# Kernel tuning notes

Hardware: AMD Instinct MI355X
Metric: run time of the kernel (lower is better)

Reference implementation:

```python
import jax, jax.numpy as jnp
import numpy as np

N = 200000
H = 128        # n_heads == input feature dim
HID = 512      # hidden_features
D_H = 512      # scaling denominator
C = 10.0       # tanh clip scale


def setup_inputs() -> dict:
    key = jax.random.key(0)
    k0, k1, k2, k3, k4, k5 = jax.random.split(key, 6)
    output = jax.random.normal(k0, (N, H), dtype=jnp.float32)
    # adjacency row: binary mask (which nodes are reachable neighbors)
    adj_modified = (jax.random.uniform(k1, (N,)) < 0.5).astype(jnp.float32)
    W1 = jax.random.normal(k2, (HID, H), dtype=jnp.float32) * (1.0 / np.sqrt(H))
    b1 = jax.random.normal(k3, (HID,), dtype=jnp.float32) * 0.01
    W2 = jax.random.normal(k4, (HID, H), dtype=jnp.float32) * (1.0 / np.sqrt(H))
    b2 = jax.random.normal(k5, (HID,), dtype=jnp.float32) * 0.01
    return {"output": output, "adj_modified": adj_modified,
            "W1": W1, "b1": b1, "W2": W2, "b2": b2, "prev_node": 5}


def reference(output, adj_modified, W1, b1, W2, b2, prev_node):
    # v_i: [1, H] embedding of the previously selected node
    v_i = output[prev_node][None, :]
    # v_j: [N, H] neighbor embeddings gated by the adjacency row
    v_j = adj_modified[:, None] * output
    phi1_v_i = v_i @ W1.T + b1          # [1, HID]
    phi2_v_j = v_j @ W2.T + b2          # [N, HID]
    scores = (phi1_v_i @ phi2_v_j.T) / jnp.sqrt(jnp.asarray(D_H, jnp.float32))  # [1, N]
    attn = C * jnp.tanh(scores) * adj_modified  # clipped + masked, [1, N]
    attn = attn[0]                                # [N]
    w = jax.nn.softmax(attn, axis=0)
    w = w * (attn != 0).astype(w.dtype)
    p = w.max()
    selected_node = jnp.argmax(w)
    return selected_node, p
```

## Files before the change

### kernel.cpp

```cpp
#include <hip/hip_runtime.h>
#include <math.h>

#define H 128
#define HID 512
#define GRID 2048
#define PREP_B 16

struct Ws {
    float sb_part[PREP_B];
    float u_part[PREP_B][H];
    unsigned long long best_part[GRID];
    float Z_part[GRID];
};

__device__ __forceinline__ unsigned int fkey(float f) {
    unsigned int u = __float_as_uint(f);
    return (u & 0x80000000u) ? ~u : (u | 0x80000000u);
}
__device__ __forceinline__ float inv_fkey(unsigned int k) {
    return __uint_as_float((k & 0x80000000u) ? (k ^ 0x80000000u) : ~k);
}

__global__ __launch_bounds__(256)
void prep_kernel(const float* __restrict__ outp, const float* __restrict__ W1,
                 const float* __restrict__ b1, const float* __restrict__ W2,
                 const float* __restrict__ b2, const int* __restrict__ prev,
                 Ws* __restrict__ ws) {
    __shared__ float phi1_s[32];
    __shared__ float sb_s[8];
    __shared__ float u_s[2][H];
    int t = threadIdx.x;
    int lane = t & 63;
    int c = lane & 31;
    int g = t >> 5;
    int kbase = blockIdx.x * 32;
    const float4* vi = (const float4*)(outp + (size_t)prev[0] * H);
    float4 v = vi[c];
    float sb = 0.f;
#pragma unroll
    for (int r = 0; r < 4; ++r) {
        int kl = g * 4 + r;
        int k = kbase + kl;
        float4 w = ((const float4*)(W1 + (size_t)k * H))[c];
        float d = w.x * v.x + w.y * v.y + w.z * v.z + w.w * v.w;
        d += __shfl_xor(d, 16);
        d += __shfl_xor(d, 8);
        d += __shfl_xor(d, 4);
        d += __shfl_xor(d, 2);
        d += __shfl_xor(d, 1);
        if (c == 0) {
            float phi = d + b1[k];
            phi1_s[kl] = phi;
            sb += phi * b2[k];
        }
    }
    if (c == 0) sb_s[g] = sb;
    __syncthreads();
    int h = t & 127;
    int g2 = t >> 7;
    float up = 0.f;
#pragma unroll
    for (int kk = 0; kk < 16; ++kk) {
        int kl = g2 * 16 + kk;
        up += phi1_s[kl] * W2[(size_t)(kbase + kl) * H + h];
    }
    u_s[g2][h] = up;
    __syncthreads();
    if (t < H) ws->u_part[blockIdx.x][t] = u_s[0][t] + u_s[1][t];
    if (t == 0) {
        float s = 0.f;
#pragma unroll
        for (int i = 0; i < 8; ++i) s += sb_s[i];
        ws->sb_part[blockIdx.x] = s;
    }
}

__global__ __launch_bounds__(256)
void score_kernel(const float4* __restrict__ xv, const float* __restrict__ adj,
                  Ws* __restrict__ ws, int n, int ntiles) {
    __shared__ float zs[4];
    __shared__ unsigned long long bs[4];
    const float inv = 0.04419417382415922f;
    int t = threadIdx.x;
    int lane = t & 63;
    int c = lane & 31;
    int hv = lane >> 5;
    int w = t >> 6;
    float4 uv = make_float4(0.f, 0.f, 0.f, 0.f);
    float s_b = 0.f;
#pragma unroll
    for (int b = 0; b < PREP_B; ++b) {
        float4 p = ((const float4*)ws->u_part[b])[c];
        uv.x += p.x; uv.y += p.y; uv.z += p.z; uv.w += p.w;
        s_b += ws->sb_part[b];
    }
    float zloc = 0.f;
    float bscore = -3.4e38f;
    int bidx = -1;
    for (int tile = blockIdx.x; tile < ntiles; tile += GRID) {
        int base = tile * 32 + w * 8 + hv;
        float4 x[4];
#pragma unroll
        for (int r = 0; r < 4; ++r) {
            int row = base + 2 * r;
            if (row >= n) row = n - 1;
            x[r] = xv[(size_t)row * 32 + c];
        }
        float d[4];
#pragma unroll
        for (int r = 0; r < 4; ++r) {
            float dd = x[r].x * uv.x + x[r].y * uv.y + x[r].z * uv.z + x[r].w * uv.w;
            dd += __shfl_xor(dd, 16);
            dd += __shfl_xor(dd, 8);
            dd += __shfl_xor(dd, 4);
            dd += __shfl_xor(dd, 2);
            dd += __shfl_xor(dd, 1);
            d[r] = dd;
        }
        if (c < 4) {
            int row = base + 2 * c;
            if (row < n) {
                float dm = d[0];
#pragma unroll
                for (int r = 1; r < 4; ++r) dm = (c == r) ? d[r] : dm;
                float a = adj[row];
                float attn = 0.f;
                if (a != 0.f) {
                    float score = (s_b + a * dm) * inv;
                    float e = __expf(2.f * score);
                    attn = 10.f * ((e - 1.f) / (e + 1.f));
                    if (score > bscore) { bscore = score; bidx = row; }
                }
                zloc += __expf(attn);
            }
        }
    }
#pragma unroll
    for (int m = 32; m >= 1; m >>= 1) zloc += __shfl_xor(zloc, m);
    unsigned long long pk = 0ull;
    if (bidx >= 0)
        pk = ((unsigned long long)fkey(bscore) << 32) |
             (unsigned long long)(0xFFFFFFFFu - (unsigned int)bidx);
#pragma unroll
    for (int m = 32; m >= 1; m >>= 1) {
        unsigned long long o = __shfl_xor(pk, m);
        if (o > pk) pk = o;
    }
    if (lane == 0) { zs[w] = zloc; bs[w] = pk; }
    __syncthreads();
    if (t == 0) {
        float z = zs[0] + zs[1] + zs[2] + zs[3];
        unsigned long long p2 = bs[0];
#pragma unroll
        for (int i = 1; i < 4; ++i) if (bs[i] > p2) p2 = bs[i];
        ws->Z_part[blockIdx.x] = z;
        ws->best_part[blockIdx.x] = p2;
    }
}

__global__ __launch_bounds__(1024)
void reduce_kernel(const Ws* __restrict__ ws, float* __restrict__ outp) {
    __shared__ float zs[16];
    __shared__ unsigned long long bs[16];
    int t = threadIdx.x;
    int lane = t & 63;
    float z = ws->Z_part[t] + ws->Z_part[t + 1024];
    unsigned long long pk = ws->best_part[t];
    unsigned long long o2 = ws->best_part[t + 1024];
    if (o2 > pk) pk = o2;
#pragma unroll
    for (int m = 32; m >= 1; m >>= 1) {
        z += __shfl_xor(z, m);
        unsigned long long o = __shfl_xor(pk, m);
        if (o > pk) pk = o;
    }
    if (lane == 0) { zs[t >> 6] = z; bs[t >> 6] = pk; }
    __syncthreads();
    if (t == 0) {
        float Z = 0.f;
        unsigned long long b = 0ull;
#pragma unroll
        for (int i = 0; i < 16; ++i) { Z += zs[i]; if (bs[i] > b) b = bs[i]; }
        unsigned int idx = 0xFFFFFFFFu - (unsigned int)(b & 0xFFFFFFFFu);
        float score = inv_fkey((unsigned int)(b >> 32));
        float p = __expf(10.f * tanhf(score)) / Z;
        if (b == 0ull) { idx = 0; p = 0.f; }
        outp[0] = (float)idx;
        outp[1] = p;
    }
}

extern "C" void kernel_launch(void* const* d_in, const int* in_sizes, int n_in,
                              void* d_out, int out_size, void* d_ws, size_t ws_size,
                              hipStream_t stream) {
    const float* outp = (const float*)d_in[0];
    const float* adj  = (const float*)d_in[1];
    const float* W1   = (const float*)d_in[2];
    const float* b1   = (const float*)d_in[3];
    const float* W2   = (const float*)d_in[4];
    const float* b2   = (const float*)d_in[5];
    const int*   prev = (const int*)d_in[6];
    int n = in_sizes[1];
    Ws* ws = (Ws*)d_ws;

    int ntiles = (n + 31) / 32;

    prep_kernel<<<PREP_B, 256, 0, stream>>>(outp, W1, b1, W2, b2, prev, ws);
    score_kernel<<<GRID, 256, 0, stream>>>((const float4*)outp, adj, ws, n, ntiles);
    reduce_kernel<<<1, 1024, 0, stream>>>(ws, (float*)d_out);
}
```

Baseline: 169.0 us.

## Fuse prep, score and reduce into one cooperative kernel with grid syncs

Merges the three launches into a single cooperative kernel of 1024 blocks that uses grid.sync between the weight-folding prep phase, the streaming score phase and the final reduction. This removes two kernel launch boundaries and their gaps. It also hoists the adjacency load ahead of the row loads and replaces exp(0) with a constant 1 for masked rows. In exchange it halves the grid size, which may reduce memory-level parallelism, and it adds the cost of grid-wide barriers.

```diff
diff --git a/kernel.cpp b/kernel.cpp
--- a/kernel.cpp
+++ b/kernel.cpp
@@ -1,16 +1,19 @@
 #include <hip/hip_runtime.h>
+#include <hip/hip_cooperative_groups.h>
 #include <math.h>
+
+namespace cg = cooperative_groups;
 
 #define H 128
 #define HID 512
-#define GRID 2048
+#define NB 1024
 #define PREP_B 16
 
 struct Ws {
     float sb_part[PREP_B];
     float u_part[PREP_B][H];
-    unsigned long long best_part[GRID];
-    float Z_part[GRID];
+    unsigned long long best_part[NB];
+    float Z_part[NB];
 };
 
 __device__ __forceinline__ unsigned int fkey(float f) {
@@ -21,71 +24,73 @@
     return __uint_as_float((k & 0x80000000u) ? (k ^ 0x80000000u) : ~k);
 }
 
-__global__ __launch_bounds__(256)
-void prep_kernel(const float* __restrict__ outp, const float* __restrict__ W1,
-                 const float* __restrict__ b1, const float* __restrict__ W2,
-                 const float* __restrict__ b2, const int* __restrict__ prev,
-                 Ws* __restrict__ ws) {
+__global__ __launch_bounds__(256, 4)
+void fused_kernel(const float* __restrict__ outp, const float* __restrict__ adj,
+                  const float* __restrict__ W1, const float* __restrict__ b1,
+                  const float* __restrict__ W2, const float* __restrict__ b2,
+                  const int* __restrict__ prev, Ws* __restrict__ ws,
+                  float* __restrict__ out, int n, int ntiles) {
     __shared__ float phi1_s[32];
     __shared__ float sb_s[8];
     __shared__ float u_s[2][H];
-    int t = threadIdx.x;
-    int lane = t & 63;
-    int c = lane & 31;
-    int g = t >> 5;
-    int kbase = blockIdx.x * 32;
-    const float4* vi = (const float4*)(outp + (size_t)prev[0] * H);
-    float4 v = vi[c];
-    float sb = 0.f;
-#pragma unroll
-    for (int r = 0; r < 4; ++r) {
-        int kl = g * 4 + r;
-        int k = kbase + kl;
-        float4 w = ((const float4*)(W1 + (size_t)k * H))[c];
-        float d = w.x * v.x + w.y * v.y + w.z * v.z + w.w * v.w;
-        d += __shfl_xor(d, 16);
-        d += __shfl_xor(d, 8);
-        d += __shfl_xor(d, 4);
-        d += __shfl_xor(d, 2);
-        d += __shfl_xor(d, 1);
-        if (c == 0) {
-            float phi = d + b1[k];
-            phi1_s[kl] = phi;
-            sb += phi * b2[k];
-        }
-    }
-    if (c == 0) sb_s[g] = sb;
-    __syncthreads();
-    int h = t & 127;
-    int g2 = t >> 7;
-    float up = 0.f;
-#pragma unroll
-    for (int kk = 0; kk < 16; ++kk) {
-        int kl = g2 * 16 + kk;
-        up += phi1_s[kl] * W2[(size_t)(kbase + kl) * H + h];
-    }
-    u_s[g2][h] = up;
-    __syncthreads();
-    if (t < H) ws->u_part[blockIdx.x][t] = u_s[0][t] + u_s[1][t];
-    if (t == 0) {
-        float s = 0.f;
-#pragma unroll
-        for (int i = 0; i < 8; ++i) s += sb_s[i];
-        ws->sb_part[blockIdx.x] = s;
-    }
-}
-
-__global__ __launch_bounds__(256)
-void score_kernel(const float4* __restrict__ xv, const float* __restrict__ adj,
-                  Ws* __restrict__ ws, int n, int ntiles) {
     __shared__ float zs[4];
     __shared__ unsigned long long bs[4];
-    const float inv = 0.04419417382415922f;
+    cg::grid_group grid = cg::this_grid();
+
     int t = threadIdx.x;
     int lane = t & 63;
     int c = lane & 31;
     int hv = lane >> 5;
     int w = t >> 6;
+    int blk = blockIdx.x;
+
+    if (blk < PREP_B) {
+        int g = t >> 5;
+        int kbase = blk * 32;
+        const float4* vi = (const float4*)(outp + (size_t)prev[0] * H);
+        float4 v = vi[c];
+        float sb = 0.f;
+#pragma unroll
+        for (int r = 0; r < 4; ++r) {
+            int kl = g * 4 + r;
+            int k = kbase + kl;
+            float4 wv = ((const float4*)(W1 + (size_t)k * H))[c];
+            float d = wv.x * v.x + wv.y * v.y + wv.z * v.z + wv.w * v.w;
+            d += __shfl_xor(d, 16);
+            d += __shfl_xor(d, 8);
+            d += __shfl_xor(d, 4);
+            d += __shfl_xor(d, 2);
+            d += __shfl_xor(d, 1);
+            if (c == 0) {
+                float phi = d + b1[k];
+                phi1_s[kl] = phi;
+                sb += phi * b2[k];
+            }
+        }
+        if (c == 0) sb_s[g] = sb;
+        __syncthreads();
+        int h = t & 127;
+        int g2 = t >> 7;
+        float up = 0.f;
+#pragma unroll
+        for (int kk = 0; kk < 16; ++kk) {
+            int kl = g2 * 16 + kk;
+            up += phi1_s[kl] * W2[(size_t)(kbase + kl) * H + h];
+        }
+        u_s[g2][h] = up;
+        __syncthreads();
+        if (t < H) ws->u_part[blk][t] = u_s[0][t] + u_s[1][t];
+        if (t == 0) {
+            float s = 0.f;
+#pragma unroll
+            for (int i = 0; i < 8; ++i) s += sb_s[i];
+            ws->sb_part[blk] = s;
+        }
+    }
+
+    grid.sync();
+
+    const float inv = 0.04419417382415922f;
     float4 uv = make_float4(0.f, 0.f, 0.f, 0.f);
     float s_b = 0.f;
 #pragma unroll
@@ -97,8 +102,12 @@
     float zloc = 0.f;
     float bscore = -3.4e38f;
     int bidx = -1;
-    for (int tile = blockIdx.x; tile < ntiles; tile += GRID) {
+    const float4* xv = (const float4*)outp;
+    for (int tile = blk; tile < ntiles; tile += NB) {
         int base = tile * 32 + w * 8 + hv;
+        float aown = 0.f;
+        int trow = base + 2 * c;
+        if (c < 4 && trow < n) aown = adj[trow];
         float4 x[4];
 #pragma unroll
         for (int r = 0; r < 4; ++r) {
@@ -117,21 +126,18 @@
             dd += __shfl_xor(dd, 1);
             d[r] = dd;
         }
-        if (c < 4) {
-            int row = base + 2 * c;
-            if (row < n) {
-                float dm = d[0];
-#pragma unroll
-                for (int r = 1; r < 4; ++r) dm = (c == r) ? d[r] : dm;
-                float a = adj[row];
-                float attn = 0.f;
-                if (a != 0.f) {
-                    float score = (s_b + a * dm) * inv;
-                    float e = __expf(2.f * score);
-                    attn = 10.f * ((e - 1.f) / (e + 1.f));
-                    if (score > bscore) { bscore = score; bidx = row; }
-                }
+        if (c < 4 && trow < n) {
+            float dm = d[0];
+#pragma unroll
+            for (int r = 1; r < 4; ++r) dm = (c == r) ? d[r] : dm;
+            if (aown != 0.f) {
+                float score = (s_b + aown * dm) * inv;
+                float e = __expf(2.f * score);
+                float attn = 10.f * ((e - 1.f) / (e + 1.f));
                 zloc += __expf(attn);
+                if (score > bscore) { bscore = score; bidx = trow; }
+            } else {
+                zloc += 1.0f;
             }
         }
     }
@@ -146,6 +152,7 @@
         unsigned long long o = __shfl_xor(pk, m);
         if (o > pk) pk = o;
     }
+    __syncthreads();
     if (lane == 0) { zs[w] = zloc; bs[w] = pk; }
     __syncthreads();
     if (t == 0) {
@@ -153,40 +160,43 @@
         unsigned long long p2 = bs[0];
 #pragma unroll
         for (int i = 1; i < 4; ++i) if (bs[i] > p2) p2 = bs[i];
-        ws->Z_part[blockIdx.x] = z;
-        ws->best_part[blockIdx.x] = p2;
-    }
-}
-
-__global__ __launch_bounds__(1024)
-void reduce_kernel(const Ws* __restrict__ ws, float* __restrict__ outp) {
-    __shared__ float zs[16];
-    __shared__ unsigned long long bs[16];
-    int t = threadIdx.x;
-    int lane = t & 63;
-    float z = ws->Z_part[t] + ws->Z_part[t + 1024];
-    unsigned long long pk = ws->best_part[t];
-    unsigned long long o2 = ws->best_part[t + 1024];
-    if (o2 > pk) pk = o2;
-#pragma unroll
-    for (int m = 32; m >= 1; m >>= 1) {
-        z += __shfl_xor(z, m);
-        unsigned long long o = __shfl_xor(pk, m);
-        if (o > pk) pk = o;
-    }
-    if (lane == 0) { zs[t >> 6] = z; bs[t >> 6] = pk; }
-    __syncthreads();
-    if (t == 0) {
-        float Z = 0.f;
-        unsigned long long b = 0ull;
-#pragma unroll
-        for (int i = 0; i < 16; ++i) { Z += zs[i]; if (bs[i] > b) b = bs[i]; }
-        unsigned int idx = 0xFFFFFFFFu - (unsigned int)(b & 0xFFFFFFFFu);
-        float score = inv_fkey((unsigned int)(b >> 32));
-        float p = __expf(10.f * tanhf(score)) / Z;
-        if (b == 0ull) { idx = 0; p = 0.f; }
-        outp[0] = (float)idx;
-        outp[1] = p;
+        ws->Z_part[blk] = z;
+        ws->best_part[blk] = p2;
+    }
+
+    grid.sync();
+
+    if (blk == 0) {
+        float z = 0.f;
+        unsigned long long pk2 = 0ull;
+#pragma unroll
+        for (int i = 0; i < 4; ++i) {
+            int s = t + 256 * i;
+            z += ws->Z_part[s];
+            unsigned long long o = ws->best_part[s];
+            if (o > pk2) pk2 = o;
+        }
+#pragma unroll
+        for (int m = 32; m >= 1; m >>= 1) {
+            z += __shfl_xor(z, m);
+            unsigned long long o = __shfl_xor(pk2, m);
+            if (o > pk2) pk2 = o;
+        }
+        __syncthreads();
+        if (lane == 0) { zs[w] = z; bs[w] = pk2; }
+        __syncthreads();
+        if (t == 0) {
+            float Z = zs[0] + zs[1] + zs[2] + zs[3];
+            unsigned long long b = bs[0];
+#pragma unroll
+            for (int i = 1; i < 4; ++i) if (bs[i] > b) b = bs[i];
+            unsigned int idx = 0xFFFFFFFFu - (unsigned int)(b & 0xFFFFFFFFu);
+            float score = inv_fkey((unsigned int)(b >> 32));
+            float p = __expf(10.f * tanhf(score)) / Z;
+            if (b == 0ull) { idx = 0; p = 0.f; }
+            out[0] = (float)idx;
+            out[1] = p;
+        }
     }
 }
 
@@ -202,10 +212,12 @@
     const int*   prev = (const int*)d_in[6];
     int n = in_sizes[1];
     Ws* ws = (Ws*)d_ws;
-
+    float* out = (float*)d_out;
     int ntiles = (n + 31) / 32;
 
-    prep_kernel<<<PREP_B, 256, 0, stream>>>(outp, W1, b1, W2, b2, prev, ws);
-    score_kernel<<<GRID, 256, 0, stream>>>((const float4*)outp, adj, ws, n, ntiles);
-    reduce_kernel<<<1, 1024, 0, stream>>>(ws, (float*)d_out);
-}
+    void* args[] = { (void*)&outp, (void*)&adj, (void*)&W1, (void*)&b1,
+                     (void*)&W2, (void*)&b2, (void*)&prev, (void*)&ws,
+                     (void*)&out, (void*)&n, (void*)&ntiles };
+    hipLaunchCooperativeKernel((const void*)fused_kernel, dim3(NB), dim3(256),
+                               args, 0, stream);
+}
```

New measurement: 400.4 us. 137% more time.
